# Kernel optimization log

Measured on AMD Instinct MI355X. Metric: run time of the kernel, lower is better.

Reference implementation:

```python
import jax, jax.numpy as jnp
import numpy as np

G = 9.8          # gravity constant from the module
B = 1024         # buckets per mid layer == spigots per bucket
M = 14           # number of homogeneous mid layers
L = M + 2        # total network layers (head bucket + mids + outlet layer)


def _solve_bucket(H0, S_b, theta_b, inflow):
    """Faithful port of solve_single_bucket.
    H0: scalar head, S_b: (n_sp, 2) [spigot height, area], theta_b: (n_sp,),
    inflow: scalar. Sequential spigot loop -> lax.scan.
    Note: after the first spigot, H_effective = H0 - cum_q/2 (inflow dropped),
    exactly as in the torch code."""
    def step(carry, x):
        H_eff, cum = carry
        sp_h, sp_a, th = x
        h = jnp.maximum(0.0, H_eff - sp_h)
        q = th * jnp.sqrt(2.0 * G * h) * sp_a
        cum = cum + q
        return (H0 - 0.5 * cum, cum), q
    init = (H0 + inflow, jnp.zeros((), S_b.dtype))
    (_, cum_q), qs = jax.lax.scan(step, init, (S_b[:, 0], S_b[:, 1], theta_b))
    H_final = H0 - cum_q + inflow
    return H_final, qs


def setup_inputs() -> dict:
    key = jax.random.key(0)
    ks = jax.random.split(key, 10)
    H0 = jax.random.uniform(ks[0], (1,), jnp.float32) * 5.0
    H_mid = jax.random.uniform(ks[1], (M, B), jnp.float32) * 5.0
    H_last = jax.random.uniform(ks[2], (B,), jnp.float32) * 5.0
    S0 = jax.random.uniform(ks[3], (1, B, 2), jnp.float32)
    S_mid = jax.random.uniform(ks[4], (M, B, B, 2), jnp.float32)
    S_last = jax.random.uniform(ks[5], (B, 1, 2), jnp.float32)
    theta0 = jax.random.uniform(ks[6], (B,), jnp.float32)
    theta_mid = jax.random.uniform(ks[7], (M, B, B), jnp.float32)
    theta_last = jax.random.uniform(ks[8], (B,), jnp.float32)
    precip = jax.random.uniform(ks[9], (), jnp.float32) * 2.0
    return {"H0": H0, "H_mid": H_mid, "H_last": H_last,
            "S0": S0, "S_mid": S_mid, "S_last": S_last,
            "theta0": theta0, "theta_mid": theta_mid, "theta_last": theta_last,
            "precip": precip}


def reference(H0, H_mid, H_last, S0, S_mid, S_last, theta0, theta_mid, theta_last, precip):
    p_layer = precip / L            # precip_inflow_per_layer ('even')
    p_bucket = p_layer / B          # per-bucket share in B-bucket layers

    # layer 0: single head bucket with B spigots, inflow = precip/L
    H0_new, q0 = _solve_bucket(H0[0], S0[0], theta0, p_layer)
    inflow = q0 + p_bucket          # inflow to each of layer-1's B buckets

    # mid layers: vmap over buckets, scan over layers (sequential dependency)
    def mid_layer(inflow, xs):
        H_l, S_l, th_l = xs         # (B,), (B,B,2), (B,B)
        Hn, q = jax.vmap(_solve_bucket)(H_l, S_l, th_l, inflow)
        return q.sum(axis=0) + p_bucket, Hn
    inflow, H_mid_new = jax.lax.scan(mid_layer, inflow, (H_mid, S_mid, theta_mid))

    # last layer: B buckets with a single outlet spigot each
    H_last_new, q_last = jax.vmap(_solve_bucket)(H_last, S_last, theta_last[:, None], inflow)

    # flat output: new heads of all layers + outlet flows
    return jnp.concatenate([H0_new[None], H_mid_new.reshape(-1), H_last_new, q_last.reshape(-1)])
```

## Files before the change

kernel.cpp:

```cpp
#include <hip/hip_runtime.h>
#include <math.h>

#define TWO_G 19.6f
#define NPART 256

__device__ __forceinline__ float flow_q(float th, float d, float a) {
    return th * sqrtf(TWO_G * d) * a;
}

__device__ __forceinline__ float wave_sum(float v) {
#pragma unroll
    for (int o = 32; o > 0; o >>= 1) v += __shfl_xor(v, o);
    return v;
}

__global__ __launch_bounds__(64)
void layer0_kernel(const float* __restrict__ H0p, const float* __restrict__ S0,
                   const float* __restrict__ theta0, const float* __restrict__ precip,
                   float* __restrict__ out, float* __restrict__ P0)
{
    const int lane = threadIdx.x;
    const float H  = H0p[0];
    const float pl = precip[0] * 0.0625f;

    const float2* S2 = (const float2*)S0;
    float2 sv[16]; float tv[16];
#pragma unroll
    for (int c = 0; c < 16; ++c) { sv[c] = S2[c * 64 + lane]; tv[c] = theta0[c * 64 + lane]; }

    float h0 = __shfl(sv[0].x, 0);
    float a0 = __shfl(sv[0].y, 0);
    float t0 = __shfl(tv[0], 0);
    float d0 = (H + pl) - h0;
    float q0 = (d0 > 0.0f) ? flow_q(t0, d0, a0) : 0.0f;
    float cum = q0;
    float u   = H - 0.5f * cum;
    if (lane == 0) P0[0] = q0;

#pragma unroll
    for (int c = 0; c < 16; ++c) {
        int i = c * 64 + lane;
        float2 s = sv[c];
        unsigned long long avail = (c == 0) ? ~1ull : ~0ull;
        unsigned long long cand  = __ballot(s.x < u) & avail;
        float qmine = 0.0f;
        while (cand) {
            int j = __builtin_ctzll(cand);
            float hj = __shfl(s.x, j);
            float aj = __shfl(s.y, j);
            float tj = __shfl(tv[c], j);
            float d = u - hj;
            float q = flow_q(tj, d, aj);
            cum += q;
            u = H - 0.5f * cum;
            if (lane == j) qmine = q;
            if (j >= 63) break;
            avail &= (~0ull << (j + 1));
            cand = __ballot(s.x < u) & avail;
        }
        if (i > 0) P0[i] = qmine;
    }
    if (lane == 0) out[0] = (H - cum) + pl;
}

__global__ __launch_bounds__(256)
void mid_kernel(const float* __restrict__ Hl, const float* __restrict__ Sl,
                const float* __restrict__ thl, const float* __restrict__ Pin,
                int npart, float* __restrict__ Pout, float* __restrict__ outl,
                const float* __restrict__ precip)
{
    __shared__ float acc[1024];
    const int tid  = threadIdx.x;
    const int lane = tid & 63;
    const int b    = blockIdx.x * 4 + (tid >> 6);

#pragma unroll
    for (int r = 0; r < 4; ++r) acc[r * 256 + tid] = 0.0f;
    __syncthreads();

    const float pb = precip[0] * (0.0625f / 1024.0f);

    float part = 0.0f;
    for (int k = lane; k < npart; k += 64) part += Pin[k * 1024 + b];

    const float2* S2   = (const float2*)Sl + (size_t)b * 1024;
    const float*  thrw = thl + (size_t)b * 1024;
    float2 sv[16]; float tv[16];
#pragma unroll
    for (int c = 0; c < 16; ++c) { sv[c] = S2[c * 64 + lane]; tv[c] = thrw[c * 64 + lane]; }

    const float H      = Hl[b];
    const float inflow = pb + wave_sum(part);

    float h0 = __shfl(sv[0].x, 0);
    float a0 = __shfl(sv[0].y, 0);
    float t0 = __shfl(tv[0], 0);
    float d0 = (H + inflow) - h0;
    float q0 = (d0 > 0.0f) ? flow_q(t0, d0, a0) : 0.0f;
    float cum = q0;
    float u   = H - 0.5f * cum;
    if (lane == 0 && q0 != 0.0f) atomicAdd(&acc[0], q0);

#pragma unroll
    for (int c = 0; c < 16; ++c) {
        float2 s = sv[c];
        unsigned long long avail = (c == 0) ? ~1ull : ~0ull;
        unsigned long long cand  = __ballot(s.x < u) & avail;
        float qmine = 0.0f;
        while (cand) {
            int j = __builtin_ctzll(cand);
            float hj = __shfl(s.x, j);
            float aj = __shfl(s.y, j);
            float tj = __shfl(tv[c], j);
            float d = u - hj;
            float q = flow_q(tj, d, aj);
            cum += q;
            u = H - 0.5f * cum;
            if (lane == j) qmine = q;
            if (j >= 63) break;
            avail &= (~0ull << (j + 1));
            cand = __ballot(s.x < u) & avail;
        }
        if (qmine != 0.0f) atomicAdd(&acc[c * 64 + lane], qmine);
    }
    if (lane == 0) outl[b] = (H - cum) + inflow;

    __syncthreads();
#pragma unroll
    for (int r = 0; r < 4; ++r)
        Pout[(size_t)blockIdx.x * 1024 + r * 256 + tid] = acc[r * 256 + tid];
}

__global__ __launch_bounds__(256)
void last_kernel(const float* __restrict__ Hlast, const float* __restrict__ Slast,
                 const float* __restrict__ thlast, const float* __restrict__ Pin,
                 const float* __restrict__ precip, float* __restrict__ out)
{
    const int lane = threadIdx.x & 63;
    const int b    = blockIdx.x * 4 + (threadIdx.x >> 6);
    const float pb = precip[0] * (0.0625f / 1024.0f);

    float part = 0.0f;
#pragma unroll
    for (int k = 0; k < NPART / 64; ++k) part += Pin[(k * 64 + lane) * 1024 + b];
    float inflow = pb + wave_sum(part);

    if (lane == 0) {
        float H = Hlast[b];
        float2 s = ((const float2*)Slast)[b];
        float d = (H + inflow) - s.x;
        float q = (d > 0.0f) ? flow_q(thlast[b], d, s.y) : 0.0f;
        out[1 + 14 * 1024 + b]        = (H - q) + inflow;
        out[1 + 14 * 1024 + 1024 + b] = q;
    }
}

extern "C" void kernel_launch(void* const* d_in, const int* in_sizes, int n_in,
                              void* d_out, int out_size, void* d_ws, size_t ws_size,
                              hipStream_t stream)
{
    (void)in_sizes; (void)n_in; (void)out_size; (void)ws_size;
    const float* H0     = (const float*)d_in[0];
    const float* Hmid   = (const float*)d_in[1];
    const float* Hlast  = (const float*)d_in[2];
    const float* S0     = (const float*)d_in[3];
    const float* Smid   = (const float*)d_in[4];
    const float* Slast  = (const float*)d_in[5];
    const float* th0    = (const float*)d_in[6];
    const float* thmid  = (const float*)d_in[7];
    const float* thlast = (const float*)d_in[8];
    const float* precip = (const float*)d_in[9];
    float* out = (float*)d_out;
    float* PA  = (float*)d_ws;
    float* PB  = PA + (size_t)NPART * 1024;

    layer0_kernel<<<1, 64, 0, stream>>>(H0, S0, th0, precip, out, PA);

    float* cur = PA;
    float* nxt = PB;
    int npart = 1;
    for (int l = 0; l < 14; ++l) {
        mid_kernel<<<256, 256, 0, stream>>>(Hmid + (size_t)l * 1024,
                                            Smid + (size_t)l * 1024 * 1024 * 2,
                                            thmid + (size_t)l * 1024 * 1024,
                                            cur, npart, nxt,
                                            out + 1 + (size_t)l * 1024,
                                            precip);
        float* t = cur; cur = nxt; nxt = t;
        npart = NPART;
    }

    last_kernel<<<256, 256, 0, stream>>>(Hlast, Slast, thlast, cur, precip, out);
}
```

Baseline: 302.2 us.

## Fuse layer cascade into one cooperative kernel with next-row prefetch

Replaces the sixteen separate kernel launches with a single cooperative kernel that uses grid.sync between layers. Each wave prefetches its next layer's spigot row into a second register set while solving the current layer, which hides global-memory latency behind the serial spigot loop. Lane broadcasts switch from __shfl to readlane. The kernel holds two 48-float register buffers and pays grid-barrier cost per layer, and it falls back to the old multi-launch path if the cooperative launch fails.

```diff
diff --git a/kernel.cpp b/kernel.cpp
--- a/kernel.cpp
+++ b/kernel.cpp
@@ -1,5 +1,8 @@
 #include <hip/hip_runtime.h>
+#include <hip/hip_cooperative_groups.h>
 #include <math.h>
+
+namespace cg = cooperative_groups;
 
 #define TWO_G 19.6f
 #define NPART 256
@@ -14,23 +17,70 @@
     return v;
 }
 
-__global__ __launch_bounds__(64)
-void layer0_kernel(const float* __restrict__ H0p, const float* __restrict__ S0,
-                   const float* __restrict__ theta0, const float* __restrict__ precip,
-                   float* __restrict__ out, float* __restrict__ P0)
-{
-    const int lane = threadIdx.x;
+__device__ __forceinline__ float lane_bcast(float v, int j) {
+    return __int_as_float(__builtin_amdgcn_readlane(__float_as_int(v), j));
+}
+
+__device__ __forceinline__ void prefetch_row(const float2* __restrict__ S2,
+                                             const float* __restrict__ th, int lane,
+                                             float2 (&sv)[16], float (&tv)[16]) {
+#pragma unroll
+    for (int c = 0; c < 16; ++c) { sv[c] = S2[c * 64 + lane]; tv[c] = th[c * 64 + lane]; }
+}
+
+__device__ __forceinline__ float solve_serial(float H, float inflow, int lane,
+                                              float2 (&sv)[16], float (&tv)[16],
+                                              float* acc) {
+    float h0 = lane_bcast(sv[0].x, 0);
+    float a0 = lane_bcast(sv[0].y, 0);
+    float t0 = lane_bcast(tv[0], 0);
+    float d0 = (H + inflow) - h0;
+    float q0 = (d0 > 0.0f) ? flow_q(t0, d0, a0) : 0.0f;
+    float cum = q0;
+    float u   = H - 0.5f * cum;
+    if (lane == 0 && q0 != 0.0f) atomicAdd(&acc[0], q0);
+
+#pragma unroll
+    for (int c = 0; c < 16; ++c) {
+        float2 s = sv[c];
+        unsigned long long avail = (c == 0) ? ~1ull : ~0ull;
+        unsigned long long cand  = __ballot(s.x < u) & avail;
+        float qmine = 0.0f;
+        while (cand) {
+            int j = __builtin_ctzll(cand);
+            float hj = lane_bcast(s.x, j);
+            float aj = lane_bcast(s.y, j);
+            float tj = lane_bcast(tv[c], j);
+            float d = u - hj;
+            float q = flow_q(tj, d, aj);
+            cum += q;
+            u = H - 0.5f * cum;
+            if (lane == j) qmine = q;
+            if (j >= 63) break;
+            avail &= (~0ull << (j + 1));
+            cand = __ballot(s.x < u) & avail;
+        }
+        if (qmine != 0.0f) atomicAdd(&acc[c * 64 + lane], qmine);
+    }
+    return cum;
+}
+
+__device__ __forceinline__ void layer0_body(const float* __restrict__ H0p,
+                                            const float* __restrict__ S0,
+                                            const float* __restrict__ theta0,
+                                            const float* __restrict__ precip,
+                                            float* __restrict__ out,
+                                            float* __restrict__ P0, int lane) {
     const float H  = H0p[0];
     const float pl = precip[0] * 0.0625f;
-
     const float2* S2 = (const float2*)S0;
     float2 sv[16]; float tv[16];
 #pragma unroll
     for (int c = 0; c < 16; ++c) { sv[c] = S2[c * 64 + lane]; tv[c] = theta0[c * 64 + lane]; }
 
-    float h0 = __shfl(sv[0].x, 0);
-    float a0 = __shfl(sv[0].y, 0);
-    float t0 = __shfl(tv[0], 0);
+    float h0 = lane_bcast(sv[0].x, 0);
+    float a0 = lane_bcast(sv[0].y, 0);
+    float t0 = lane_bcast(tv[0], 0);
     float d0 = (H + pl) - h0;
     float q0 = (d0 > 0.0f) ? flow_q(t0, d0, a0) : 0.0f;
     float cum = q0;
@@ -46,9 +96,9 @@
         float qmine = 0.0f;
         while (cand) {
             int j = __builtin_ctzll(cand);
-            float hj = __shfl(s.x, j);
-            float aj = __shfl(s.y, j);
-            float tj = __shfl(tv[c], j);
+            float hj = lane_bcast(s.x, j);
+            float aj = lane_bcast(s.y, j);
+            float tj = lane_bcast(tv[c], j);
             float d = u - hj;
             float q = flow_q(tj, d, aj);
             cum += q;
@@ -63,6 +113,107 @@
     if (lane == 0) out[0] = (H - cum) + pl;
 }
 
+__device__ __forceinline__ void mid_step(int l, int b, int lane, int tid, int bid,
+                                         const float* __restrict__ Hmid, float pb,
+                                         float2 (&sv)[16], float (&tv)[16],
+                                         float2 (&svn)[16], float (&tvn)[16],
+                                         const float2* __restrict__ Sn,
+                                         const float* __restrict__ thn, bool doPrefetch,
+                                         const float* __restrict__ Pin, bool firstLayer,
+                                         float* __restrict__ Pout, float* __restrict__ out,
+                                         float* acc, cg::grid_group& grid) {
+    float part = 0.0f;
+    if (firstLayer) {
+        if (lane == 0) part = Pin[b];
+    } else {
+#pragma unroll
+        for (int k = 0; k < 4; ++k) part += Pin[(size_t)(k * 64 + lane) * 1024 + b];
+    }
+    if (doPrefetch) prefetch_row(Sn, thn, lane, svn, tvn);
+
+    const float H      = Hmid[(size_t)l * 1024 + b];
+    const float inflow = pb + wave_sum(part);
+    const float cum    = solve_serial(H, inflow, lane, sv, tv, acc);
+    if (lane == 0) out[1 + (size_t)l * 1024 + b] = (H - cum) + inflow;
+
+    __syncthreads();
+#pragma unroll
+    for (int r = 0; r < 4; ++r) {
+        const int idx = r * 256 + tid;
+        Pout[(size_t)bid * 1024 + idx] = acc[idx];
+        acc[idx] = 0.0f;
+    }
+    grid.sync();
+}
+
+__global__ __launch_bounds__(256, 1)
+void cascade_kernel(const float* __restrict__ H0p, const float* __restrict__ Hmid,
+                    const float* __restrict__ Hlast, const float* __restrict__ S0,
+                    const float* __restrict__ Smid, const float* __restrict__ Slast,
+                    const float* __restrict__ th0, const float* __restrict__ thmid,
+                    const float* __restrict__ thlast, const float* __restrict__ precip,
+                    float* __restrict__ out, float* __restrict__ PA, float* __restrict__ PB)
+{
+    cg::grid_group grid = cg::this_grid();
+    __shared__ float acc[1024];
+    const int tid  = threadIdx.x;
+    const int lane = tid & 63;
+    const int bid  = blockIdx.x;
+    const int b    = bid * 4 + (tid >> 6);
+
+#pragma unroll
+    for (int r = 0; r < 4; ++r) acc[r * 256 + tid] = 0.0f;
+
+    const float pb = precip[0] * (0.0625f / 1024.0f);
+    const float2* S2m = (const float2*)Smid;
+
+    float2 svA[16]; float tvA[16];
+    float2 svB[16]; float tvB[16];
+
+    prefetch_row(S2m + (size_t)b * 1024, thmid + (size_t)b * 1024, lane, svA, tvA);
+
+    if (bid == 0 && tid < 64)
+        layer0_body(H0p, S0, th0, precip, out, PA, lane);
+
+    grid.sync();
+
+#pragma unroll 1
+    for (int l = 0; l < 14; l += 2) {
+        mid_step(l, b, lane, tid, bid, Hmid, pb, svA, tvA, svB, tvB,
+                 S2m + ((size_t)(l + 1) * 1024 * 1024 + (size_t)b * 1024),
+                 thmid + ((size_t)(l + 1) * 1024 * 1024 + (size_t)b * 1024),
+                 true, PA, l == 0, PB, out, acc, grid);
+        const bool  pf  = (l + 2) < 14;
+        const size_t off = pf ? ((size_t)(l + 2) * 1024 * 1024 + (size_t)b * 1024)
+                              : ((size_t)b * 1024);
+        mid_step(l + 1, b, lane, tid, bid, Hmid, pb, svB, tvB, svA, tvA,
+                 S2m + off, thmid + off, pf, PB, false, PA, out, acc, grid);
+    }
+
+    {
+        float part = 0.0f;
+#pragma unroll
+        for (int k = 0; k < 4; ++k) part += PA[(size_t)(k * 64 + lane) * 1024 + b];
+        const float inflow = pb + wave_sum(part);
+        if (lane == 0) {
+            const float  Hv = Hlast[b];
+            const float2 s  = ((const float2*)Slast)[b];
+            const float  d  = (Hv + inflow) - s.x;
+            const float  q  = (d > 0.0f) ? flow_q(thlast[b], d, s.y) : 0.0f;
+            out[1 + 14 * 1024 + b]        = (Hv - q) + inflow;
+            out[1 + 14 * 1024 + 1024 + b] = q;
+        }
+    }
+}
+
+__global__ __launch_bounds__(64)
+void layer0_kernel(const float* __restrict__ H0p, const float* __restrict__ S0,
+                   const float* __restrict__ theta0, const float* __restrict__ precip,
+                   float* __restrict__ out, float* __restrict__ P0)
+{
+    layer0_body(H0p, S0, theta0, precip, out, P0, threadIdx.x);
+}
+
 __global__ __launch_bounds__(256)
 void mid_kernel(const float* __restrict__ Hl, const float* __restrict__ Sl,
                 const float* __restrict__ thl, const float* __restrict__ Pin,
@@ -81,48 +232,14 @@
     const float pb = precip[0] * (0.0625f / 1024.0f);
 
     float part = 0.0f;
-    for (int k = lane; k < npart; k += 64) part += Pin[k * 1024 + b];
-
-    const float2* S2   = (const float2*)Sl + (size_t)b * 1024;
-    const float*  thrw = thl + (size_t)b * 1024;
+    for (int k = lane; k < npart; k += 64) part += Pin[(size_t)k * 1024 + b];
+
     float2 sv[16]; float tv[16];
-#pragma unroll
-    for (int c = 0; c < 16; ++c) { sv[c] = S2[c * 64 + lane]; tv[c] = thrw[c * 64 + lane]; }
+    prefetch_row((const float2*)Sl + (size_t)b * 1024, thl + (size_t)b * 1024, lane, sv, tv);
 
     const float H      = Hl[b];
     const float inflow = pb + wave_sum(part);
-
-    float h0 = __shfl(sv[0].x, 0);
-    float a0 = __shfl(sv[0].y, 0);
-    float t0 = __shfl(tv[0], 0);
-    float d0 = (H + inflow) - h0;
-    float q0 = (d0 > 0.0f) ? flow_q(t0, d0, a0) : 0.0f;
-    float cum = q0;
-    float u   = H - 0.5f * cum;
-    if (lane == 0 && q0 != 0.0f) atomicAdd(&acc[0], q0);
-
-#pragma unroll
-    for (int c = 0; c < 16; ++c) {
-        float2 s = sv[c];
-        unsigned long long avail = (c == 0) ? ~1ull : ~0ull;
-        unsigned long long cand  = __ballot(s.x < u) & avail;
-        float qmine = 0.0f;
-        while (cand) {
-            int j = __builtin_ctzll(cand);
-            float hj = __shfl(s.x, j);
-            float aj = __shfl(s.y, j);
-            float tj = __shfl(tv[c], j);
-            float d = u - hj;
-            float q = flow_q(tj, d, aj);
-            cum += q;
-            u = H - 0.5f * cum;
-            if (lane == j) qmine = q;
-            if (j >= 63) break;
-            avail &= (~0ull << (j + 1));
-            cand = __ballot(s.x < u) & avail;
-        }
-        if (qmine != 0.0f) atomicAdd(&acc[c * 64 + lane], qmine);
-    }
+    const float cum    = solve_serial(H, inflow, lane, sv, tv, acc);
     if (lane == 0) outl[b] = (H - cum) + inflow;
 
     __syncthreads();
@@ -142,7 +259,7 @@
 
     float part = 0.0f;
 #pragma unroll
-    for (int k = 0; k < NPART / 64; ++k) part += Pin[(k * 64 + lane) * 1024 + b];
+    for (int k = 0; k < NPART / 64; ++k) part += Pin[(size_t)(k * 64 + lane) * 1024 + b];
     float inflow = pb + wave_sum(part);
 
     if (lane == 0) {
@@ -174,21 +291,21 @@
     float* PA  = (float*)d_ws;
     float* PB  = PA + (size_t)NPART * 1024;
 
-    layer0_kernel<<<1, 64, 0, stream>>>(H0, S0, th0, precip, out, PA);
-
-    float* cur = PA;
-    float* nxt = PB;
-    int npart = 1;
-    for (int l = 0; l < 14; ++l) {
-        mid_kernel<<<256, 256, 0, stream>>>(Hmid + (size_t)l * 1024,
-                                            Smid + (size_t)l * 1024 * 1024 * 2,
-                                            thmid + (size_t)l * 1024 * 1024,
-                                            cur, npart, nxt,
-                                            out + 1 + (size_t)l * 1024,
-                                            precip);
-        float* t = cur; cur = nxt; nxt = t;
-        npart = NPART;
-    }
-
-    last_kernel<<<256, 256, 0, stream>>>(Hlast, Slast, thlast, cur, precip, out);
-}
+    void* args[] = { &H0, &Hmid, &Hlast, &S0, &Smid, &Slast,
+                     &th0, &thmid, &thlast, &precip, &out, &PA, &PB };
+    hipError_t err = hipLaunchCooperativeKernel((const void*)cascade_kernel,
+                                                dim3(256), dim3(256), args, 0, stream);
+    if (err != hipSuccess) {
+        layer0_kernel<<<1, 64, 0, stream>>>(H0, S0, th0, precip, out, PA);
+        float* cur = PA; float* nxt = PB; int npart = 1;
+        for (int l = 0; l < 14; ++l) {
+            mid_kernel<<<256, 256, 0, stream>>>(Hmid + (size_t)l * 1024,
+                                                Smid + (size_t)l * 1024 * 1024 * 2,
+                                                thmid + (size_t)l * 1024 * 1024,
+                                                cur, npart, nxt,
+                                                out + 1 + (size_t)l * 1024, precip);
+            float* t = cur; cur = nxt; nxt = t; npart = NPART;
+        }
+        last_kernel<<<256, 256, 0, stream>>>(Hlast, Slast, thlast, cur, precip, out);
+    }
+}
```

Result: slower. 721.6 us (+138.8%).
